# Performance work log

Measured on AMD Instinct MI355X. Metric: run time of the kernel, lower is better.

## Reference

```python
import jax, jax.numpy as jnp
import numpy as np


def setup_inputs() -> dict:
    key = jax.random.key(0)
    k1, k2, k3 = jax.random.split(key, 3)
    n, c, h, w = 32, 384, 56, 56
    m, d_model = 8, 768
    x = jax.random.normal(k1, (n, c, h, w), dtype=jnp.float32)
    global_feature = jax.random.normal(k2, (n, m, d_model), dtype=jnp.float32)
    # Linear(d_model, 2*c): torch weight shape (2c, d_model)
    W_kv = jax.random.normal(k3, (2 * c, d_model), dtype=jnp.float32) * (1.0 / np.sqrt(d_model))
    b_kv = jnp.zeros((2 * c,), dtype=jnp.float32)
    return {"x": x, "global_feature": global_feature, "W_kv": W_kv, "b_kv": b_kv}


def reference(x, global_feature, W_kv, b_kv):
    n, c, h, w = x.shape
    # MLP (single Linear + ReLU6, no BN since bn=False)
    kv = jnp.einsum('nmd,ed->nme', global_feature, W_kv) + b_kv  # [n, m, 2c]
    kv = jnp.clip(kv, 0.0, 6.0)  # ReLU6
    K = kv[:, :, :c]   # [n, m, c]
    V = kv[:, :, c:]   # [n, m, c]
    q = x.reshape(n, c, h * w).transpose(0, 2, 1)  # [n, hw, c]
    scores = jnp.einsum('nqc,nkc->nqk', q, K)       # [n, hw, m] (unscaled)
    attn = jax.nn.softmax(scores, axis=-1)
    v_agg = jnp.einsum('nqk,nkc->nqc', attn, V)     # [n, hw, c]
    feature = v_agg.transpose(0, 2, 1).reshape(n, c, h, w)
    return feature + x
```

## Files before the change

### kernel.cpp

```cpp
#include <hip/hip_runtime.h>


#define NC 384
#define HWP 3136
#define DD 768
#define MM 8
#define EE 768

__global__ __launch_bounds__(256) void kv_kernel(const float* __restrict__ gf,
                                                 const float* __restrict__ Wk,
                                                 const float* __restrict__ bk,
                                                 float* __restrict__ kv) {
    __shared__ float g[MM * DD];
    const int n = blockIdx.y;
    const int et = blockIdx.x;
    const int t = threadIdx.x;

    const float* gfn = gf + (size_t)n * (MM * DD);
    for (int i = t; i < MM * DD; i += 256) g[i] = gfn[i];
    __syncthreads();

    const int e = et * 64 + (t & 63);
    const int mb = (t >> 6) * 2;

    const float4* w4 = (const float4*)(Wk + (size_t)e * DD);
    const float4* g0 = (const float4*)(g + (mb + 0) * DD);
    const float4* g1 = (const float4*)(g + (mb + 1) * DD);

    float a0 = 0.f, a1 = 0.f;
    #pragma unroll 8
    for (int i = 0; i < DD / 4; ++i) {
        const float4 w = w4[i];
        const float4 v0 = g0[i];
        const float4 v1 = g1[i];
        a0 += w.x * v0.x + w.y * v0.y + w.z * v0.z + w.w * v0.w;
        a1 += w.x * v1.x + w.y * v1.y + w.z * v1.z + w.w * v1.w;
    }
    const float bv = bk[e];
    float* o = kv + (size_t)n * (MM * EE);
    o[(mb + 0) * EE + e] = fminf(fmaxf(a0 + bv, 0.f), 6.f);
    o[(mb + 1) * EE + e] = fminf(fmaxf(a1 + bv, 0.f), 6.f);
}

__global__ __launch_bounds__(256) void attn_kernel(const float* __restrict__ x,
                                                   const float* __restrict__ kv,
                                                   float* __restrict__ out) {
    __shared__ float kvs[MM * EE];
    __shared__ float sc[4][8][64];
    __shared__ float attn_s[8][64];

    const int n = blockIdx.y;
    const int tile = blockIdx.x;
    const int t = threadIdx.x;
    const int p4 = t & 15;
    const int g = t >> 4;
    const int w = t >> 6;
    const int pos0 = tile * 64 + p4 * 4;
    const int c0 = g * 24;

    const float4* kvn4 = (const float4*)(kv + (size_t)n * (MM * EE));
    float4* kvs4 = (float4*)kvs;
    for (int i = t; i < MM * EE / 4; i += 256) kvs4[i] = kvn4[i];

    const float* xp = x + (size_t)n * NC * HWP + (size_t)c0 * HWP + pos0;
    float4 xr[24];
    #pragma unroll
    for (int i = 0; i < 24; ++i) xr[i] = *(const float4*)(xp + (size_t)i * HWP);

    __syncthreads();

    float acc[8][4];
    #pragma unroll
    for (int k = 0; k < 8; ++k)
        #pragma unroll
        for (int j = 0; j < 4; ++j) acc[k][j] = 0.f;

    #pragma unroll
    for (int i = 0; i < 24; ++i) {
        const float4 xv = xr[i];
        #pragma unroll
        for (int k = 0; k < 8; ++k) {
            const float kc = kvs[k * EE + c0 + i];
            acc[k][0] += xv.x * kc;
            acc[k][1] += xv.y * kc;
            acc[k][2] += xv.z * kc;
            acc[k][3] += xv.w * kc;
        }
    }

    #pragma unroll
    for (int k = 0; k < 8; ++k) {
        #pragma unroll
        for (int j = 0; j < 4; ++j) {
            acc[k][j] += __shfl_xor(acc[k][j], 16, 64);
            acc[k][j] += __shfl_xor(acc[k][j], 32, 64);
        }
    }
    if ((t & 48) == 0) {
        #pragma unroll
        for (int k = 0; k < 8; ++k) {
            *(float4*)&sc[w][k][p4 * 4] =
                make_float4(acc[k][0], acc[k][1], acc[k][2], acc[k][3]);
        }
    }
    __syncthreads();

    if (t < 64) {
        float s[8];
        float mx = -1e30f;
        #pragma unroll
        for (int k = 0; k < 8; ++k) {
            s[k] = sc[0][k][t] + sc[1][k][t] + sc[2][k][t] + sc[3][k][t];
            mx = fmaxf(mx, s[k]);
        }
        float sum = 0.f;
        #pragma unroll
        for (int k = 0; k < 8; ++k) {
            s[k] = __expf(s[k] - mx);
            sum += s[k];
        }
        const float inv = 1.f / sum;
        #pragma unroll
        for (int k = 0; k < 8; ++k) attn_s[k][t] = s[k] * inv;
    }
    __syncthreads();

    float4 aw[8];
    #pragma unroll
    for (int k = 0; k < 8; ++k) aw[k] = *(const float4*)&attn_s[k][p4 * 4];

    float* op = out + (size_t)n * NC * HWP + (size_t)c0 * HWP + pos0;
    #pragma unroll
    for (int i = 0; i < 24; ++i) {
        float4 o = xr[i];
        #pragma unroll
        for (int k = 0; k < 8; ++k) {
            const float v = kvs[k * EE + 384 + c0 + i];
            o.x += aw[k].x * v;
            o.y += aw[k].y * v;
            o.z += aw[k].z * v;
            o.w += aw[k].w * v;
        }
        *(float4*)(op + (size_t)i * HWP) = o;
    }
}

extern "C" void kernel_launch(void* const* d_in, const int* in_sizes, int n_in,
                              void* d_out, int out_size, void* d_ws, size_t ws_size,
                              hipStream_t stream) {
    const float* x  = (const float*)d_in[0];
    const float* gf = (const float*)d_in[1];
    const float* Wk = (const float*)d_in[2];
    const float* bk = (const float*)d_in[3];
    float* out = (float*)d_out;
    float* kv = (float*)d_ws;

    kv_kernel<<<dim3(12, 32), 256, 0, stream>>>(gf, Wk, bk, kv);
    attn_kernel<<<dim3(49, 32), 256, 0, stream>>>(x, kv, out);
}
```

Baseline: 321.6 us.

## Remap threads so each wavefront owns positions and reduces channels via shuffles

Threads are remapped so that each wavefront covers 16 positions, with its 64 lanes split into 16 channel groups of 24 channels. The channel reduction now runs entirely through wavefront shuffles, and the softmax is computed in registers, which removes the shared-memory score staging and two block barriers. K/V are stored in shared memory with a padded stride of 25 per group to avoid bank conflicts. In exchange, global memory accesses become less contiguous: each 4-lane group reads only 64 bytes per channel row. The staging loop also does integer divisions, and every lane now computes the softmax redundantly.

Result: slower. 333.6 us (+3.7%).

```diff
diff --git a/kernel.cpp b/kernel.cpp
--- a/kernel.cpp
+++ b/kernel.cpp
@@ -45,22 +45,28 @@
 __global__ __launch_bounds__(256) void attn_kernel(const float* __restrict__ x,
                                                    const float* __restrict__ kv,
                                                    float* __restrict__ out) {
-    __shared__ float kvs[MM * EE];
-    __shared__ float sc[4][8][64];
-    __shared__ float attn_s[8][64];
+    __shared__ float kvs[6400];
 
     const int n = blockIdx.y;
     const int tile = blockIdx.x;
     const int t = threadIdx.x;
-    const int p4 = t & 15;
-    const int g = t >> 4;
+    const int lane = t & 63;
     const int w = t >> 6;
-    const int pos0 = tile * 64 + p4 * 4;
+    const int q = lane & 3;
+    const int g = lane >> 2;
     const int c0 = g * 24;
+    const int pos0 = tile * 64 + w * 16 + q * 4;
 
-    const float4* kvn4 = (const float4*)(kv + (size_t)n * (MM * EE));
-    float4* kvs4 = (float4*)kvs;
-    for (int i = t; i < MM * EE / 4; i += 256) kvs4[i] = kvn4[i];
+    const float* kvn = kv + (size_t)n * (MM * EE);
+    for (int idx = t; idx < MM * EE; idx += 256) {
+        const int k = idx / EE;
+        const int e = idx - k * EE;
+        const int half = (e >= 384) ? 1 : 0;
+        const int c = e - half * 384;
+        const int gg = c / 24;
+        const int j = c - gg * 24;
+        kvs[half * 3200 + k * 400 + gg * 25 + j] = kvn[idx];
+    }
 
     const float* xp = x + (size_t)n * NC * HWP + (size_t)c0 * HWP + pos0;
     float4 xr[24];
@@ -80,7 +86,7 @@
         const float4 xv = xr[i];
         #pragma unroll
         for (int k = 0; k < 8; ++k) {
-            const float kc = kvs[k * EE + c0 + i];
+            const float kc = kvs[k * 400 + g * 25 + i];
             acc[k][0] += xv.x * kc;
             acc[k][1] += xv.y * kc;
             acc[k][2] += xv.z * kc;
@@ -92,42 +98,32 @@
     for (int k = 0; k < 8; ++k) {
         #pragma unroll
         for (int j = 0; j < 4; ++j) {
-            acc[k][j] += __shfl_xor(acc[k][j], 16, 64);
-            acc[k][j] += __shfl_xor(acc[k][j], 32, 64);
+            float v = acc[k][j];
+            v += __shfl_xor(v, 4, 64);
+            v += __shfl_xor(v, 8, 64);
+            v += __shfl_xor(v, 16, 64);
+            v += __shfl_xor(v, 32, 64);
+            acc[k][j] = v;
         }
     }
-    if ((t & 48) == 0) {
+
+    float aw[8][4];
+    #pragma unroll
+    for (int j = 0; j < 4; ++j) {
+        float mx = acc[0][j];
         #pragma unroll
-        for (int k = 0; k < 8; ++k) {
-            *(float4*)&sc[w][k][p4 * 4] =
-                make_float4(acc[k][0], acc[k][1], acc[k][2], acc[k][3]);
-        }
-    }
-    __syncthreads();
-
-    if (t < 64) {
-        float s[8];
-        float mx = -1e30f;
-        #pragma unroll
-        for (int k = 0; k < 8; ++k) {
-            s[k] = sc[0][k][t] + sc[1][k][t] + sc[2][k][t] + sc[3][k][t];
-            mx = fmaxf(mx, s[k]);
-        }
+        for (int k = 1; k < 8; ++k) mx = fmaxf(mx, acc[k][j]);
         float sum = 0.f;
         #pragma unroll
         for (int k = 0; k < 8; ++k) {
-            s[k] = __expf(s[k] - mx);
-            sum += s[k];
+            const float e = __expf(acc[k][j] - mx);
+            aw[k][j] = e;
+            sum += e;
         }
         const float inv = 1.f / sum;
         #pragma unroll
-        for (int k = 0; k < 8; ++k) attn_s[k][t] = s[k] * inv;
+        for (int k = 0; k < 8; ++k) aw[k][j] *= inv;
     }
-    __syncthreads();
-
-    float4 aw[8];
-    #pragma unroll
-    for (int k = 0; k < 8; ++k) aw[k] = *(const float4*)&attn_s[k][p4 * 4];
 
     float* op = out + (size_t)n * NC * HWP + (size_t)c0 * HWP + pos0;
     #pragma unroll
@@ -135,11 +131,11 @@
         float4 o = xr[i];
         #pragma unroll
         for (int k = 0; k < 8; ++k) {
-            const float v = kvs[k * EE + 384 + c0 + i];
-            o.x += aw[k].x * v;
-            o.y += aw[k].y * v;
-            o.z += aw[k].z * v;
-            o.w += aw[k].w * v;
+            const float v = kvs[3200 + k * 400 + g * 25 + i];
+            o.x += aw[k][0] * v;
+            o.y += aw[k][1] * v;
+            o.z += aw[k][2] * v;
+            o.w += aw[k][3] * v;
         }
         *(float4*)(op + (size_t)i * HWP) = o;
     }
```

## Halve attention tile width, pad shared KV layout, compute softmax redundantly per thread

Applied to the files above, without the earlier changes.

The attention kernel now has each thread handle two positions instead of four, so the grid doubles and each block covers 32 positions. Per-thread x registers shrink, and launch bounds request four blocks per SM for higher occupancy. The shared KV buffer is repacked into a padded per-group layout so K and V can be read as float4 with fewer bank conflicts. Every thread now computes the softmax for its own positions, which removes the single-wave softmax stage and one barrier. The cost is redundant softmax work, more blocks, and twice as many KV shared-memory fills across the grid.

Result: no change. 319.7 us (-0.6%).

```diff
diff --git a/kernel.cpp b/kernel.cpp
--- a/kernel.cpp
+++ b/kernel.cpp
@@ -42,106 +42,118 @@
     o[(mb + 1) * EE + e] = fminf(fmaxf(a1 + bv, 0.f), 6.f);
 }
 
-__global__ __launch_bounds__(256) void attn_kernel(const float* __restrict__ x,
-                                                   const float* __restrict__ kv,
-                                                   float* __restrict__ out) {
-    __shared__ float kvs[MM * EE];
-    __shared__ float sc[4][8][64];
-    __shared__ float attn_s[8][64];
+__global__ __launch_bounds__(256, 4) void attn_kernel(const float* __restrict__ x,
+                                                      const float* __restrict__ kv,
+                                                      float* __restrict__ out) {
+    __shared__ float kvs[7168];
+    __shared__ float sc[4][8][32];
 
     const int n = blockIdx.y;
     const int tile = blockIdx.x;
     const int t = threadIdx.x;
-    const int p4 = t & 15;
-    const int g = t >> 4;
+    const int p2 = t & 15;
+    const int gq = t >> 4;
     const int w = t >> 6;
-    const int pos0 = tile * 64 + p4 * 4;
-    const int c0 = g * 24;
+    const int c0 = gq * 24;
+    const int pos0 = tile * 32 + p2 * 2;
 
     const float4* kvn4 = (const float4*)(kv + (size_t)n * (MM * EE));
-    float4* kvs4 = (float4*)kvs;
-    for (int i = t; i < MM * EE / 4; i += 256) kvs4[i] = kvn4[i];
+    #pragma unroll
+    for (int r = 0; r < 6; ++r) {
+        const int f = t + r * 256;
+        const int k = f / 192;
+        const int e4 = f - k * 192;
+        const int half = (e4 >= 96) ? 1 : 0;
+        const int c4 = e4 - half * 96;
+        const int g = c4 / 6;
+        const int j4 = c4 - g * 6;
+        *(float4*)&kvs[half * 3584 + k * 448 + g * 28 + j4 * 4] = kvn4[f];
+    }
 
     const float* xp = x + (size_t)n * NC * HWP + (size_t)c0 * HWP + pos0;
-    float4 xr[24];
+    float2 xr[24];
     #pragma unroll
-    for (int i = 0; i < 24; ++i) xr[i] = *(const float4*)(xp + (size_t)i * HWP);
+    for (int i = 0; i < 24; ++i) xr[i] = *(const float2*)(xp + (size_t)i * HWP);
 
     __syncthreads();
 
-    float acc[8][4];
+    float accx[8], accy[8];
     #pragma unroll
-    for (int k = 0; k < 8; ++k)
-        #pragma unroll
-        for (int j = 0; j < 4; ++j) acc[k][j] = 0.f;
+    for (int k = 0; k < 8; ++k) { accx[k] = 0.f; accy[k] = 0.f; }
 
     #pragma unroll
-    for (int i = 0; i < 24; ++i) {
-        const float4 xv = xr[i];
+    for (int i4 = 0; i4 < 6; ++i4) {
+        const float2 x0 = xr[i4 * 4 + 0];
+        const float2 x1 = xr[i4 * 4 + 1];
+        const float2 x2 = xr[i4 * 4 + 2];
+        const float2 x3 = xr[i4 * 4 + 3];
         #pragma unroll
         for (int k = 0; k < 8; ++k) {
-            const float kc = kvs[k * EE + c0 + i];
-            acc[k][0] += xv.x * kc;
-            acc[k][1] += xv.y * kc;
-            acc[k][2] += xv.z * kc;
-            acc[k][3] += xv.w * kc;
+            const float4 kk = *(const float4*)&kvs[k * 448 + gq * 28 + i4 * 4];
+            accx[k] += x0.x * kk.x + x1.x * kk.y + x2.x * kk.z + x3.x * kk.w;
+            accy[k] += x0.y * kk.x + x1.y * kk.y + x2.y * kk.z + x3.y * kk.w;
         }
     }
 
     #pragma unroll
     for (int k = 0; k < 8; ++k) {
-        #pragma unroll
-        for (int j = 0; j < 4; ++j) {
-            acc[k][j] += __shfl_xor(acc[k][j], 16, 64);
-            acc[k][j] += __shfl_xor(acc[k][j], 32, 64);
-        }
+        accx[k] += __shfl_xor(accx[k], 16, 64);
+        accx[k] += __shfl_xor(accx[k], 32, 64);
+        accy[k] += __shfl_xor(accy[k], 16, 64);
+        accy[k] += __shfl_xor(accy[k], 32, 64);
     }
     if ((t & 48) == 0) {
         #pragma unroll
-        for (int k = 0; k < 8; ++k) {
-            *(float4*)&sc[w][k][p4 * 4] =
-                make_float4(acc[k][0], acc[k][1], acc[k][2], acc[k][3]);
-        }
+        for (int k = 0; k < 8; ++k)
+            *(float2*)&sc[w][k][p2 * 2] = make_float2(accx[k], accy[k]);
     }
     __syncthreads();
 
-    if (t < 64) {
-        float s[8];
-        float mx = -1e30f;
+    float sx[8], sy[8];
+    #pragma unroll
+    for (int k = 0; k < 8; ++k) {
+        float2 s = *(const float2*)&sc[0][k][p2 * 2];
+        #pragma unroll
+        for (int ww = 1; ww < 4; ++ww) {
+            const float2 q = *(const float2*)&sc[ww][k][p2 * 2];
+            s.x += q.x; s.y += q.y;
+        }
+        sx[k] = s.x; sy[k] = s.y;
+    }
+    {
+        float mx = sx[0], my = sy[0];
+        #pragma unroll
+        for (int k = 1; k < 8; ++k) { mx = fmaxf(mx, sx[k]); my = fmaxf(my, sy[k]); }
+        float sux = 0.f, suy = 0.f;
         #pragma unroll
         for (int k = 0; k < 8; ++k) {
-            s[k] = sc[0][k][t] + sc[1][k][t] + sc[2][k][t] + sc[3][k][t];
-            mx = fmaxf(mx, s[k]);
+            sx[k] = __expf(sx[k] - mx); sux += sx[k];
+            sy[k] = __expf(sy[k] - my); suy += sy[k];
         }
-        float sum = 0.f;
+        const float ix = 1.f / sux, iy = 1.f / suy;
         #pragma unroll
-        for (int k = 0; k < 8; ++k) {
-            s[k] = __expf(s[k] - mx);
-            sum += s[k];
-        }
-        const float inv = 1.f / sum;
-        #pragma unroll
-        for (int k = 0; k < 8; ++k) attn_s[k][t] = s[k] * inv;
+        for (int k = 0; k < 8; ++k) { sx[k] *= ix; sy[k] *= iy; }
     }
-    __syncthreads();
-
-    float4 aw[8];
-    #pragma unroll
-    for (int k = 0; k < 8; ++k) aw[k] = *(const float4*)&attn_s[k][p4 * 4];
 
     float* op = out + (size_t)n * NC * HWP + (size_t)c0 * HWP + pos0;
     #pragma unroll
-    for (int i = 0; i < 24; ++i) {
-        float4 o = xr[i];
+    for (int i4 = 0; i4 < 6; ++i4) {
+        float2 o0 = xr[i4 * 4 + 0];
+        float2 o1 = xr[i4 * 4 + 1];
+        float2 o2 = xr[i4 * 4 + 2];
+        float2 o3 = xr[i4 * 4 + 3];
         #pragma unroll
         for (int k = 0; k < 8; ++k) {
-            const float v = kvs[k * EE + 384 + c0 + i];
-            o.x += aw[k].x * v;
-            o.y += aw[k].y * v;
-            o.z += aw[k].z * v;
-            o.w += aw[k].w * v;
+            const float4 vv = *(const float4*)&kvs[3584 + k * 448 + gq * 28 + i4 * 4];
+            o0.x += sx[k] * vv.x; o0.y += sy[k] * vv.x;
+            o1.x += sx[k] * vv.y; o1.y += sy[k] * vv.y;
+            o2.x += sx[k] * vv.z; o2.y += sy[k] * vv.z;
+            o3.x += sx[k] * vv.w; o3.y += sy[k] * vv.w;
         }
-        *(float4*)(op + (size_t)i * HWP) = o;
+        *(float2*)(op + (size_t)(i4 * 4 + 0) * HWP) = o0;
+        *(float2*)(op + (size_t)(i4 * 4 + 1) * HWP) = o1;
+        *(float2*)(op + (size_t)(i4 * 4 + 2) * HWP) = o2;
+        *(float2*)(op + (size_t)(i4 * 4 + 3) * HWP) = o3;
     }
 }
 
@@ -156,5 +168,5 @@
     float* kv = (float*)d_ws;
 
     kv_kernel<<<dim3(12, 32), 256, 0, stream>>>(gf, Wk, bk, kv);
-    attn_kernel<<<dim3(49, 32), 256, 0, stream>>>(x, kv, out);
+    attn_kernel<<<dim3(98, 32), 256, 0, stream>>>(x, kv, out);
 }
```
